# Kernel optimization log

Measured on AMD Instinct MI355X. Metric: run time of the kernel, lower is better.

## Reference

```python
import jax, jax.numpy as jnp
import numpy as np

B, NB, K, C, CM, POS = 8, 1024, 9, 32, 128, 2
SIGMA = 0.5
NEG_SLOPE = 0.01  # nn.LeakyReLU default
BN_EPS = 1e-5


def _leaky(x):
    return jnp.where(x >= 0, x, NEG_SLOPE * x)


def _batchnorm(x, gamma, beta):
    # BatchNorm1d, training-mode batch statistics over the point dimension
    mu = jnp.mean(x, axis=0)
    var = jnp.mean((x - mu) ** 2, axis=0)
    return gamma * (x - mu) * jax.lax.rsqrt(var + BN_EPS) + beta


def setup_inputs() -> dict:
    key = jax.random.key(0)
    ks = jax.random.split(key, 8)
    N = B * NB
    positions = jax.random.normal(ks[0], (N, POS), jnp.float32)
    weights = jax.random.normal(ks[1], (N, C), jnp.float32)
    batch = jnp.full((B,), NB, dtype=jnp.int32)  # uniform point counts per graph
    # KernelConv params: kernel_init='grid' -> 3x3 grid of offsets spanning +-sigma
    g = jnp.linspace(-SIGMA, SIGMA, 3, dtype=jnp.float32)
    kernel_positions = jnp.stack(jnp.meshgrid(g, g, indexing='ij'), axis=-1).reshape(K, POS)
    kernel_weights = (jax.random.normal(ks[2], (K, C, C), jnp.float32) / np.float32(np.sqrt(C * K)))
    conv_norm_gamma = jnp.ones((C,), jnp.float32)
    conv_norm_beta = jnp.zeros((C,), jnp.float32)
    # PyG MLP([C, CM, C+POS], act_first=True, plain_last=True)
    W1 = jax.random.normal(ks[3], (C, CM), jnp.float32) / np.float32(np.sqrt(C))
    b1 = jnp.zeros((CM,), jnp.float32)
    bn_gamma = jnp.ones((CM,), jnp.float32)
    bn_beta = jnp.zeros((CM,), jnp.float32)
    W2 = jax.random.normal(ks[4], (CM, C + POS), jnp.float32) / np.float32(np.sqrt(CM))
    b2 = jnp.zeros((C + POS,), jnp.float32)
    return dict(positions=positions, weights=weights, batch=batch,
                kernel_positions=kernel_positions, kernel_weights=kernel_weights,
                conv_norm_gamma=conv_norm_gamma, conv_norm_beta=conv_norm_beta,
                W1=W1, b1=b1, bn_gamma=bn_gamma, bn_beta=bn_beta, W2=W2, b2=b2)


def reference(positions, weights, batch, kernel_positions, kernel_weights,
              conv_norm_gamma, conv_norm_beta, W1, b1, bn_gamma, bn_beta, W2, b2):
    N = positions.shape[0]
    # --- KernelConv: each point spawns K components at pos + kernel offset ---
    conv_pos = (positions[:, None, :] + kernel_positions[None, :, :])  # [N,K,2]
    conv_w = jnp.einsum('nc,kcd->nkd', weights, kernel_weights)        # [N,K,C]
    conv_pos = conv_pos.reshape(B, NB * K, POS)
    conv_w = conv_w.reshape(B, NB * K, C)
    # --- KernelSample: evaluate Gaussian mixture at original positions ---
    p = positions.reshape(B, NB, POS)
    d2 = (jnp.sum(p * p, -1)[:, :, None]
          + jnp.sum(conv_pos * conv_pos, -1)[:, None, :]
          - 2.0 * jnp.einsum('bnd,bmd->bnm', p, conv_pos))             # [B,NB,NB*K]
    Kmat = jnp.exp(-d2 / (2.0 * SIGMA * SIGMA))
    sampled = jnp.einsum('bnm,bmc->bnc', Kmat, conv_w).reshape(N, C)
    x = _leaky(sampled)                                                 # KernelSample nonlinearity
    # conv_norm + residual add of input weights
    x = _batchnorm(x, conv_norm_gamma, conv_norm_beta) + weights
    # MLP: lin -> act -> batchnorm (act_first) -> plain last lin
    h = _batchnorm(_leaky(x @ W1 + b1), bn_gamma, bn_beta)
    mlp_out = h @ W2 + b2                                               # [N, POS + C]
    delta_pos, delta_w = mlp_out[:, :POS], mlp_out[:, POS:]
    return positions + delta_pos, x + delta_w
```

## Files before the change

### kernel.cpp

```cpp
#include <hip/hip_runtime.h>
#include <hip/hip_bf16.h>

#define BB    8
#define NBB   1024
#define KK    9
#define CC    32
#define CMM   128
#define NTOT  (BB*NBB)
#define MM    (NBB*KK)
#define NEG   0.01f
#define EPS   1e-5f
#define SQL2  1.6986436f

#define OFF_CWT   0
#define SZ_CWT    (BB*CC*MM/2)
#define OFF_QPX   (OFF_CWT + SZ_CWT)
#define OFF_QPY   (OFF_QPX + BB*MM)
#define OFF_X0    (OFF_QPY + BB*MM)
#define OFF_X     (OFF_X0 + NTOT*CC)
#define OFF_H0    (OFF_X + NTOT*CC)
#define OFF_ST    (OFF_H0 + NTOT*CMM)

typedef __attribute__((ext_vector_type(8))) short short8;
typedef __attribute__((ext_vector_type(4))) float f32x4;
typedef __attribute__((ext_vector_type(2))) float f32x2;

static __device__ __forceinline__ unsigned short f2bf_rne(float f) {
    __hip_bfloat16 h = __float2bfloat16(f);
    return *reinterpret_cast<unsigned short*>(&h);
}


__global__ __launch_bounds__(256) void k_convw(const float* __restrict__ pos,
                                               const float* __restrict__ kpos,
                                               const float* __restrict__ w,
                                               const float* __restrict__ kw,
                                               float* __restrict__ qpx,
                                               float* __restrict__ qpy,
                                               float* __restrict__ stats,
                                               short* __restrict__ cwT) {
    __shared__ unsigned short kwl[KK*CC*CC];
    __shared__ unsigned short tile[9*32*32];
    int t = threadIdx.x;
    int l = t & 63, wv = t >> 6;
    int lane15 = l & 15, quad = l >> 4;
    int blk = blockIdx.x;
    int b = blk & 7, nbl = blk >> 3;

    if (blk == 0 && t < 320) stats[t] = 0.f;
    #pragma unroll
    for (int rep = 0; rep < 2; ++rep) {
        int gid = rep*65536 + blk*256 + t;
        if (gid < BB*MM) {
            int bb = gid / MM;
            int m = gid - bb*MM;
            int np = m / 9, k9 = m - np*9;
            float qx = pos[((size_t)(bb*NBB + np))*2 + 0] + kpos[k9*2 + 0];
            float qy = pos[((size_t)(bb*NBB + np))*2 + 1] + kpos[k9*2 + 1];
            qpx[gid] = SQL2*qx;
            qpy[gid] = SQL2*qy;
        }
    }
    for (int u = t; u < KK*CC*CC/4; u += 256) {
        int flat = u*4;
        int row = flat >> 5;
        int c0 = flat & 31;
        int kk = row >> 5, cp = row & 31;
        f32x4 v = *(const f32x4*)&kw[flat];
        kwl[(kk*CC + c0+0)*CC + cp] = f2bf_rne(v.x);
        kwl[(kk*CC + c0+1)*CC + cp] = f2bf_rne(v.y);
        kwl[(kk*CC + c0+2)*CC + cp] = f2bf_rne(v.z);
        kwl[(kk*CC + c0+3)*CC + cp] = f2bf_rne(v.w);
    }
    int n = b*NBB + nbl*32 + (wv & 1)*16 + lane15;
    f32x4 w0 = *(const f32x4*)&w[(size_t)n*CC + quad*8];
    f32x4 w1 = *(const f32x4*)&w[(size_t)n*CC + quad*8 + 4];
    union { unsigned short us[8]; short8 s; } bfr;
    bfr.us[0] = f2bf_rne(w0.x); bfr.us[1] = f2bf_rne(w0.y);
    bfr.us[2] = f2bf_rne(w0.z); bfr.us[3] = f2bf_rne(w0.w);
    bfr.us[4] = f2bf_rne(w1.x); bfr.us[5] = f2bf_rne(w1.y);
    bfr.us[6] = f2bf_rne(w1.z); bfr.us[7] = f2bf_rne(w1.w);
    __syncthreads();
    {
        int ntile = wv & 1, cth = wv >> 1;
        f32x4 acc[KK];
        #pragma unroll
        for (int kk = 0; kk < KK; ++kk) {
            int c = cth*16 + lane15;
            short8 afr = *(const short8*)&kwl[(kk*CC + c)*CC + quad*8];
            acc[kk] = __builtin_amdgcn_mfma_f32_16x16x32_bf16(
                afr, bfr.s, (f32x4)0.f, 0, 0, 0);
        }
        #pragma unroll
        for (int kk = 0; kk < KK; ++kk) {
            int ml = (ntile*16 + lane15)*9 + kk;
            unsigned short* tw = &tile[(ml >> 5)*1024 + (ml & 31)];
            #pragma unroll
            for (int reg = 0; reg < 4; ++reg) {
                int c = cth*16 + quad*4 + reg;
                tw[c*32] = f2bf_rne(acc[kk][reg]);
            }
        }
    }
    __syncthreads();
    short* dst = cwT + (size_t)b*CC*MM + (size_t)nbl*9216;
    #pragma unroll
    for (int it = 0; it < 5; ++it) {
        int u = it*256 + t;
        if (u < 1152) {
            short8 v = *(const short8*)&tile[u*8];
            *(short8*)&dst[u*8] = v;
        }
    }
}

#define LOADSET(A0,A1,XX0,XX1,YY0,YY1,it) do { \
    int _i = (it) < 18 ? (it) : 17; \
    int _m = wvm + _i*32; \
    int _a = _i*1024; \
    A0 = *(const short8*)&cab[_a]; \
    A1 = *(const short8*)&cab[_a + 512]; \
    XX0 = *(const f32x4*)&qx[_m]; XX1 = *(const f32x4*)&qx[_m + 4]; \
    YY0 = *(const f32x4*)&qy[_m]; YY1 = *(const f32x4*)&qy[_m + 4]; \
} while (0)

#define COMPUTE(A0,A1,XX0,XX1,YY0,YY1) do { \
    _Pragma("unroll") \
    for (int nt = 0; nt < 2; ++nt) { \
        f32x2 PX = {px[nt], px[nt]}; \
        f32x2 PY = {py[nt], py[nt]}; \
        f32x2 dx0 = (f32x2){XX0.x, XX0.y} - PX; \
        f32x2 dy0 = (f32x2){YY0.x, YY0.y} - PY; \
        f32x2 t0 = dx0*dx0; t0 = dy0*dy0 + t0; \
        f32x2 dx1 = (f32x2){XX0.z, XX0.w} - PX; \
        f32x2 dy1 = (f32x2){YY0.z, YY0.w} - PY; \
        f32x2 t1 = dx1*dx1; t1 = dy1*dy1 + t1; \
        f32x2 dx2 = (f32x2){XX1.x, XX1.y} - PX; \
        f32x2 dy2 = (f32x2){YY1.x, YY1.y} - PY; \
        f32x2 t2 = dx2*dx2; t2 = dy2*dy2 + t2; \
        f32x2 dx3 = (f32x2){XX1.z, XX1.w} - PX; \
        f32x2 dy3 = (f32x2){YY1.z, YY1.w} - PY; \
        f32x2 t3 = dx3*dx3; t3 = dy3*dy3 + t3; \
        float e0 = __builtin_amdgcn_exp2f(-t0.x); \
        float e1 = __builtin_amdgcn_exp2f(-t0.y); \
        float e2 = __builtin_amdgcn_exp2f(-t1.x); \
        float e3 = __builtin_amdgcn_exp2f(-t1.y); \
        float e4 = __builtin_amdgcn_exp2f(-t2.x); \
        float e5 = __builtin_amdgcn_exp2f(-t2.y); \
        float e6 = __builtin_amdgcn_exp2f(-t3.x); \
        float e7 = __builtin_amdgcn_exp2f(-t3.y); \
        union { unsigned int u[4]; short8 s; } bf; \
        bf.u[0] = __builtin_amdgcn_perm(__float_as_uint(e1), __float_as_uint(e0), 0x07060302u); \
        bf.u[1] = __builtin_amdgcn_perm(__float_as_uint(e3), __float_as_uint(e2), 0x07060302u); \
        bf.u[2] = __builtin_amdgcn_perm(__float_as_uint(e5), __float_as_uint(e4), 0x07060302u); \
        bf.u[3] = __builtin_amdgcn_perm(__float_as_uint(e7), __float_as_uint(e6), 0x07060302u); \
        acc[nt][0] = __builtin_amdgcn_mfma_f32_16x16x32_bf16(A0, bf.s, acc[nt][0], 0, 0, 0); \
        acc[nt][1] = __builtin_amdgcn_mfma_f32_16x16x32_bf16(A1, bf.s, acc[nt][1], 0, 0, 0); \
    } \
} while (0)

__global__ __launch_bounds__(1024, 4) void k_sample(const float* __restrict__ pos,
                                                    const float* __restrict__ qpx,
                                                    const float* __restrict__ qpy,
                                                    const short* __restrict__ cwT,
                                                    float* __restrict__ x0,
                                                    float* __restrict__ s1) {
    __shared__ float red[16*32*36];
    __shared__ float sstat[64];
    int t = threadIdx.x;
    int l = t & 63, wv = t >> 6;
    int blk = blockIdx.x;
    int b = blk & 7, nblk = blk >> 3;
    int lane15 = l & 15, quad = l >> 4;
    int nbase = b*NBB + nblk*32;
    if (t < 64) sstat[t] = 0.f;

    float px[2], py[2];
    #pragma unroll
    for (int nt = 0; nt < 2; ++nt) {
        int n = nbase + nt*16 + lane15;
        px[nt] = SQL2*pos[(size_t)n*2];
        py[nt] = SQL2*pos[(size_t)n*2 + 1];
    }
    f32x4 acc[2][2];
    acc[0][0] = (f32x4)0.f; acc[0][1] = (f32x4)0.f;
    acc[1][0] = (f32x4)0.f; acc[1][1] = (f32x4)0.f;

    const float* qx = qpx + (size_t)b*MM;
    const float* qy = qpy + (size_t)b*MM;
    const short* cab = cwT + (size_t)b*CC*MM + (size_t)(wv*18)*1024
                     + (size_t)lane15*32 + quad*8;
    const int wvm = wv*576 + quad*8;

    short8 a0A, a1A, a0B, a1B, a0C, a1C;
    f32x4 X0A, X1A, Y0A, Y1A, X0B, X1B, Y0B, Y1B, X0C, X1C, Y0C, Y1C;
    LOADSET(a0A, a1A, X0A, X1A, Y0A, Y1A, 0);
    LOADSET(a0B, a1B, X0B, X1B, Y0B, Y1B, 1);
    LOADSET(a0C, a1C, X0C, X1C, Y0C, Y1C, 2);
    for (int i = 0; i < 6; ++i) {
        int base = i*3;
        COMPUTE(a0A, a1A, X0A, X1A, Y0A, Y1A);
        LOADSET(a0A, a1A, X0A, X1A, Y0A, Y1A, base + 3);
        COMPUTE(a0B, a1B, X0B, X1B, Y0B, Y1B);
        LOADSET(a0B, a1B, X0B, X1B, Y0B, Y1B, base + 4);
        COMPUTE(a0C, a1C, X0C, X1C, Y0C, Y1C);
        LOADSET(a0C, a1C, X0C, X1C, Y0C, Y1C, base + 5);
    }
    #pragma unroll
    for (int nt = 0; nt < 2; ++nt)
        #pragma unroll
        for (int ct = 0; ct < 2; ++ct) {
            int nn = nt*16 + lane15, c = ct*16 + quad*4;
            *(f32x4*)&red[(wv*32 + nn)*36 + c] = acc[nt][ct];
        }
    __syncthreads();
    if (t < 256) {
        int nr = t >> 3, c0 = (t & 7)*4;
        f32x4 v = (f32x4)0.f;
        #pragma unroll
        for (int wp = 0; wp < 16; ++wp)
            v = v + *(const f32x4*)&red[(wp*32 + nr)*36 + c0];
        v.x = v.x >= 0.f ? v.x : NEG*v.x;
        v.y = v.y >= 0.f ? v.y : NEG*v.y;
        v.z = v.z >= 0.f ? v.z : NEG*v.z;
        v.w = v.w >= 0.f ? v.w : NEG*v.w;
        *(f32x4*)&x0[((size_t)(nbase + nr))*CC + c0] = v;
        float s0 = v.x, s1v = v.y, s2v = v.z, s3v = v.w;
        float q0 = v.x*v.x, q1 = v.y*v.y, q2 = v.z*v.z, q3 = v.w*v.w;
        #pragma unroll
        for (int mk = 8; mk <= 32; mk <<= 1) {
            s0 += __shfl_xor(s0, mk); s1v += __shfl_xor(s1v, mk);
            s2v += __shfl_xor(s2v, mk); s3v += __shfl_xor(s3v, mk);
            q0 += __shfl_xor(q0, mk); q1 += __shfl_xor(q1, mk);
            q2 += __shfl_xor(q2, mk); q3 += __shfl_xor(q3, mk);
        }
        if (l < 8) {
            atomicAdd(&sstat[c0 + 0], s0);  atomicAdd(&sstat[c0 + 1], s1v);
            atomicAdd(&sstat[c0 + 2], s2v); atomicAdd(&sstat[c0 + 3], s3v);
            atomicAdd(&sstat[32 + c0 + 0], q0); atomicAdd(&sstat[32 + c0 + 1], q1);
            atomicAdd(&sstat[32 + c0 + 2], q2); atomicAdd(&sstat[32 + c0 + 3], q3);
        }
    }
    __syncthreads();
    if (t < 64) atomicAdd(&s1[t], sstat[t]);
}

__global__ __launch_bounds__(256) void k_mlp1(const float* __restrict__ x0,
                                              const float* __restrict__ wts,
                                              const float* __restrict__ gma,
                                              const float* __restrict__ bta,
                                              const float* __restrict__ W1,
                                              const float* __restrict__ b1,
                                              const float* __restrict__ s1,
                                              float* __restrict__ x,
                                              float* __restrict__ h0,
                                              float* __restrict__ s2) {
    __shared__ float tile[32*68];
    int t = threadIdx.x;
    int l = t & 63, wv = t >> 6;
    int blk = blockIdx.x;
    int nb = blk >> 2, jq = blk & 3;
    int n = nb*64 + l;
    int j0 = jq*32 + wv*8;

    float xv[32];
    #pragma unroll
    for (int c = 0; c < 32; ++c) {
        float mu  = s1[c] * (1.f/NTOT);
        float var = s1[32+c]*(1.f/NTOT) - mu*mu;
        float a   = gma[c] * rsqrtf(var + EPS);
        float v   = x0[(size_t)n*CC + c];
        xv[c] = a*(v - mu) + bta[c] + wts[(size_t)n*CC + c];
    }
    if (jq == 0 && wv == 0) {
        #pragma unroll
        for (int c = 0; c < 32; c += 4)
            *(float4*)&x[(size_t)n*CC + c] = make_float4(xv[c], xv[c+1], xv[c+2], xv[c+3]);
    }
    float acc[8];
    *(f32x4*)&acc[0] = *(const f32x4*)&b1[j0];
    *(f32x4*)&acc[4] = *(const f32x4*)&b1[j0 + 4];
    #pragma unroll 8
    for (int c = 0; c < 32; ++c) {
        float xc = xv[c];
        const float* w1r = W1 + c*CMM + j0;
        f32x4 wa = *(const f32x4*)&w1r[0];
        f32x4 wb = *(const f32x4*)&w1r[4];
        acc[0] = fmaf(xc, wa.x, acc[0]); acc[1] = fmaf(xc, wa.y, acc[1]);
        acc[2] = fmaf(xc, wa.z, acc[2]); acc[3] = fmaf(xc, wa.w, acc[3]);
        acc[4] = fmaf(xc, wb.x, acc[4]); acc[5] = fmaf(xc, wb.y, acc[5]);
        acc[6] = fmaf(xc, wb.z, acc[6]); acc[7] = fmaf(xc, wb.w, acc[7]);
    }
    #pragma unroll
    for (int jj = 0; jj < 8; ++jj) {
        acc[jj] = acc[jj] >= 0.f ? acc[jj] : NEG*acc[jj];
        tile[(wv*8 + jj)*68 + l] = acc[jj];
    }
    float* hd = h0 + (size_t)n*CMM + j0;
    *(float4*)&hd[0] = make_float4(acc[0], acc[1], acc[2], acc[3]);
    *(float4*)&hd[4] = make_float4(acc[4], acc[5], acc[6], acc[7]);
    __syncthreads();
    if (t < 256) {
        int jl = t >> 3, grp = t & 7;
        float lsum = 0.f, lsq = 0.f;
        #pragma unroll
        for (int q = 0; q < 2; ++q) {
            f32x4 v = *(const f32x4*)&tile[jl*68 + grp*8 + q*4];
            lsum += v.x + v.y + v.z + v.w;
            lsq = fmaf(v.x, v.x, fmaf(v.y, v.y, fmaf(v.z, v.z, fmaf(v.w, v.w, lsq))));
        }
        lsum += __shfl_xor(lsum, 1); lsq += __shfl_xor(lsq, 1);
        lsum += __shfl_xor(lsum, 2); lsq += __shfl_xor(lsq, 2);
        lsum += __shfl_xor(lsum, 4); lsq += __shfl_xor(lsq, 4);
        if (grp == 0) {
            int jg = jq*32 + jl;
            atomicAdd(&s2[jg], lsum);
            atomicAdd(&s2[CMM + jg], lsq);
        }
    }
}

__global__ __launch_bounds__(256) void k_mlp2(const float* __restrict__ h0,
                                              const float* __restrict__ x,
                                              const float* __restrict__ pos,
                                              const float* __restrict__ g2,
                                              const float* __restrict__ bt2,
                                              const float* __restrict__ W2,
                                              const float* __restrict__ b2,
                                              const float* __restrict__ s2,
                                              float* __restrict__ out) {
    __shared__ float red[16*16*35];
    int t = threadIdx.x;
    int nl = t & 15, rid = t >> 4;
    int n = blockIdx.x*16 + nl;
    int j0 = rid*8;
    float hv[8];
    *(f32x4*)&hv[0] = *(const f32x4*)&h0[(size_t)n*CMM + j0];
    *(f32x4*)&hv[4] = *(const f32x4*)&h0[(size_t)n*CMM + j0 + 4];
    #pragma unroll
    for (int jj = 0; jj < 8; ++jj) {
        int j = j0 + jj;
        float mu  = s2[j] * (1.f/NTOT);
        float var = s2[CMM+j]*(1.f/NTOT) - mu*mu;
        float a   = g2[j] * rsqrtf(var + EPS);
        hv[jj] = a*(hv[jj] - mu) + bt2[j];
    }
    float acc[34];
    #pragma unroll
    for (int c = 0; c < 34; ++c) acc[c] = 0.f;
    for (int jj = 0; jj < 8; ++jj) {
        float h = hv[jj];
        const float* w2r = W2 + (size_t)(j0 + jj)*34;
        #pragma unroll
        for (int c = 0; c < 34; ++c)
            acc[c] = fmaf(h, w2r[c], acc[c]);
    }
    #pragma unroll
    for (int c = 0; c < 34; ++c) red[(rid*16 + nl)*35 + c] = acc[c];
    __syncthreads();
    #pragma unroll
    for (int it = 0; it < 3; ++it) {
        int u = it*256 + t;
        if (u < 544) {
            int r = u / 34, c = u - r*34;
            float v = b2[c];
            #pragma unroll
            for (int rr = 0; rr < 16; ++rr) v += red[(rr*16 + r)*35 + c];
            int nn = blockIdx.x*16 + r;
            if (c < 2)
                out[(size_t)nn*2 + c] = pos[(size_t)nn*2 + c] + v;
            else
                out[16384 + (size_t)nn*32 + (c-2)] = x[(size_t)nn*32 + (c-2)] + v;
        }
    }
}

extern "C" void kernel_launch(void* const* d_in, const int* in_sizes, int n_in,
                              void* d_out, int out_size, void* d_ws, size_t ws_size,
                              hipStream_t stream) {
    const float* positions = (const float*)d_in[0];
    const float* weights   = (const float*)d_in[1];
    const float* kpos = (const float*)d_in[3];
    const float* kw   = (const float*)d_in[4];
    const float* cg   = (const float*)d_in[5];
    const float* cb   = (const float*)d_in[6];
    const float* W1   = (const float*)d_in[7];
    const float* b1   = (const float*)d_in[8];
    const float* bg   = (const float*)d_in[9];
    const float* bb   = (const float*)d_in[10];
    const float* W2   = (const float*)d_in[11];
    const float* b2   = (const float*)d_in[12];
    float* ws  = (float*)d_ws;
    float* out = (float*)d_out;

    float* s1 = ws + OFF_ST;
    float* s2 = ws + OFF_ST + 64;

    k_convw<<<256, 256, 0, stream>>>(positions, kpos, weights, kw,
                                     ws + OFF_QPX, ws + OFF_QPY,
                                     s1, (short*)(ws + OFF_CWT));
    k_sample<<<256, 1024, 0, stream>>>(positions, ws + OFF_QPX, ws + OFF_QPY,
                                       (const short*)(ws + OFF_CWT),
                                       ws + OFF_X0, s1);
    k_mlp1<<<512, 256, 0, stream>>>(ws + OFF_X0, weights, cg, cb, W1, b1,
                                    s1, ws + OFF_X, ws + OFF_H0, s2);
    k_mlp2<<<512, 256, 0, stream>>>(ws + OFF_H0, ws + OFF_X, positions,
                                    bg, bb, W2, b2, s2, out);
}
```

Measured before the change: 145.0 us.

## Fuse four kernels into two using software grid barriers

Merges the conv-weight precompute into the sampling kernel and the two MLP kernels into one, separated by a hand-rolled atomic grid barrier. This removes two kernel launches and their launch gaps. In exchange it depends on every block being co-resident (256 blocks of 1024 threads, and 512 blocks of 256), since the barrier deadlocks otherwise. The spin-wait also adds some cost.

```diff
diff --git a/kernel.cpp b/kernel.cpp
--- a/kernel.cpp
+++ b/kernel.cpp
@@ -30,89 +30,27 @@
     return *reinterpret_cast<unsigned short*>(&h);
 }
 
-
-__global__ __launch_bounds__(256) void k_convw(const float* __restrict__ pos,
-                                               const float* __restrict__ kpos,
-                                               const float* __restrict__ w,
-                                               const float* __restrict__ kw,
-                                               float* __restrict__ qpx,
-                                               float* __restrict__ qpy,
-                                               float* __restrict__ stats,
-                                               short* __restrict__ cwT) {
-    __shared__ unsigned short kwl[KK*CC*CC];
-    __shared__ unsigned short tile[9*32*32];
-    int t = threadIdx.x;
-    int l = t & 63, wv = t >> 6;
-    int lane15 = l & 15, quad = l >> 4;
-    int blk = blockIdx.x;
-    int b = blk & 7, nbl = blk >> 3;
-
-    if (blk == 0 && t < 320) stats[t] = 0.f;
-    #pragma unroll
-    for (int rep = 0; rep < 2; ++rep) {
-        int gid = rep*65536 + blk*256 + t;
-        if (gid < BB*MM) {
-            int bb = gid / MM;
-            int m = gid - bb*MM;
-            int np = m / 9, k9 = m - np*9;
-            float qx = pos[((size_t)(bb*NBB + np))*2 + 0] + kpos[k9*2 + 0];
-            float qy = pos[((size_t)(bb*NBB + np))*2 + 1] + kpos[k9*2 + 1];
-            qpx[gid] = SQL2*qx;
-            qpy[gid] = SQL2*qy;
-        }
-    }
-    for (int u = t; u < KK*CC*CC/4; u += 256) {
-        int flat = u*4;
-        int row = flat >> 5;
-        int c0 = flat & 31;
-        int kk = row >> 5, cp = row & 31;
-        f32x4 v = *(const f32x4*)&kw[flat];
-        kwl[(kk*CC + c0+0)*CC + cp] = f2bf_rne(v.x);
-        kwl[(kk*CC + c0+1)*CC + cp] = f2bf_rne(v.y);
-        kwl[(kk*CC + c0+2)*CC + cp] = f2bf_rne(v.z);
-        kwl[(kk*CC + c0+3)*CC + cp] = f2bf_rne(v.w);
-    }
-    int n = b*NBB + nbl*32 + (wv & 1)*16 + lane15;
-    f32x4 w0 = *(const f32x4*)&w[(size_t)n*CC + quad*8];
-    f32x4 w1 = *(const f32x4*)&w[(size_t)n*CC + quad*8 + 4];
-    union { unsigned short us[8]; short8 s; } bfr;
-    bfr.us[0] = f2bf_rne(w0.x); bfr.us[1] = f2bf_rne(w0.y);
-    bfr.us[2] = f2bf_rne(w0.z); bfr.us[3] = f2bf_rne(w0.w);
-    bfr.us[4] = f2bf_rne(w1.x); bfr.us[5] = f2bf_rne(w1.y);
-    bfr.us[6] = f2bf_rne(w1.z); bfr.us[7] = f2bf_rne(w1.w);
+__device__ unsigned g_cnt[2];
+__device__ unsigned g_gen[2];
+
+static __device__ __forceinline__ void grid_sync(int i, unsigned nblk) {
+    __threadfence();
     __syncthreads();
-    {
-        int ntile = wv & 1, cth = wv >> 1;
-        f32x4 acc[KK];
-        #pragma unroll
-        for (int kk = 0; kk < KK; ++kk) {
-            int c = cth*16 + lane15;
-            short8 afr = *(const short8*)&kwl[(kk*CC + c)*CC + quad*8];
-            acc[kk] = __builtin_amdgcn_mfma_f32_16x16x32_bf16(
-                afr, bfr.s, (f32x4)0.f, 0, 0, 0);
-        }
-        #pragma unroll
-        for (int kk = 0; kk < KK; ++kk) {
-            int ml = (ntile*16 + lane15)*9 + kk;
-            unsigned short* tw = &tile[(ml >> 5)*1024 + (ml & 31)];
-            #pragma unroll
-            for (int reg = 0; reg < 4; ++reg) {
-                int c = cth*16 + quad*4 + reg;
-                tw[c*32] = f2bf_rne(acc[kk][reg]);
-            }
+    if (threadIdx.x == 0) {
+        unsigned g = __hip_atomic_load(&g_gen[i], __ATOMIC_RELAXED, __HIP_MEMORY_SCOPE_AGENT);
+        unsigned a = __hip_atomic_fetch_add(&g_cnt[i], 1u, __ATOMIC_ACQ_REL, __HIP_MEMORY_SCOPE_AGENT);
+        if (a == nblk - 1u) {
+            __hip_atomic_store(&g_cnt[i], 0u, __ATOMIC_RELAXED, __HIP_MEMORY_SCOPE_AGENT);
+            __hip_atomic_store(&g_gen[i], g + 1u, __ATOMIC_RELEASE, __HIP_MEMORY_SCOPE_AGENT);
+        } else {
+            while (__hip_atomic_load(&g_gen[i], __ATOMIC_ACQUIRE, __HIP_MEMORY_SCOPE_AGENT) == g)
+                __builtin_amdgcn_s_sleep(2);
         }
     }
     __syncthreads();
-    short* dst = cwT + (size_t)b*CC*MM + (size_t)nbl*9216;
-    #pragma unroll
-    for (int it = 0; it < 5; ++it) {
-        int u = it*256 + t;
-        if (u < 1152) {
-            short8 v = *(const short8*)&tile[u*8];
-            *(short8*)&dst[u*8] = v;
-        }
-    }
+    __threadfence();
 }
+
 
 #define LOADSET(A0,A1,XX0,XX1,YY0,YY1,it) do { \
     int _i = (it) < 18 ? (it) : 17; \
@@ -159,218 +97,299 @@
     } \
 } while (0)
 
-__global__ __launch_bounds__(1024, 4) void k_sample(const float* __restrict__ pos,
-                                                    const float* __restrict__ qpx,
-                                                    const float* __restrict__ qpy,
-                                                    const short* __restrict__ cwT,
-                                                    float* __restrict__ x0,
-                                                    float* __restrict__ s1) {
+__global__ __launch_bounds__(1024, 4) void k_cs(const float* __restrict__ pos,
+                                                const float* __restrict__ kpos,
+                                                const float* __restrict__ w,
+                                                const float* __restrict__ kw,
+                                                float* __restrict__ qpx,
+                                                float* __restrict__ qpy,
+                                                const short* __restrict__ cwTr,
+                                                short* __restrict__ cwT,
+                                                float* __restrict__ x0,
+                                                float* __restrict__ stats) {
     __shared__ float red[16*32*36];
     __shared__ float sstat[64];
+    unsigned short* kwl  = (unsigned short*)red;
+    unsigned short* tile = (unsigned short*)red + 9216;
+
     int t = threadIdx.x;
     int l = t & 63, wv = t >> 6;
     int blk = blockIdx.x;
     int b = blk & 7, nblk = blk >> 3;
     int lane15 = l & 15, quad = l >> 4;
-    int nbase = b*NBB + nblk*32;
     if (t < 64) sstat[t] = 0.f;
 
-    float px[2], py[2];
-    #pragma unroll
-    for (int nt = 0; nt < 2; ++nt) {
-        int n = nbase + nt*16 + lane15;
-        px[nt] = SQL2*pos[(size_t)n*2];
-        py[nt] = SQL2*pos[(size_t)n*2 + 1];
-    }
-    f32x4 acc[2][2];
-    acc[0][0] = (f32x4)0.f; acc[0][1] = (f32x4)0.f;
-    acc[1][0] = (f32x4)0.f; acc[1][1] = (f32x4)0.f;
-
-    const float* qx = qpx + (size_t)b*MM;
-    const float* qy = qpy + (size_t)b*MM;
-    const short* cab = cwT + (size_t)b*CC*MM + (size_t)(wv*18)*1024
-                     + (size_t)lane15*32 + quad*8;
-    const int wvm = wv*576 + quad*8;
-
-    short8 a0A, a1A, a0B, a1B, a0C, a1C;
-    f32x4 X0A, X1A, Y0A, Y1A, X0B, X1B, Y0B, Y1B, X0C, X1C, Y0C, Y1C;
-    LOADSET(a0A, a1A, X0A, X1A, Y0A, Y1A, 0);
-    LOADSET(a0B, a1B, X0B, X1B, Y0B, Y1B, 1);
-    LOADSET(a0C, a1C, X0C, X1C, Y0C, Y1C, 2);
-    for (int i = 0; i < 6; ++i) {
-        int base = i*3;
-        COMPUTE(a0A, a1A, X0A, X1A, Y0A, Y1A);
-        LOADSET(a0A, a1A, X0A, X1A, Y0A, Y1A, base + 3);
-        COMPUTE(a0B, a1B, X0B, X1B, Y0B, Y1B);
-        LOADSET(a0B, a1B, X0B, X1B, Y0B, Y1B, base + 4);
-        COMPUTE(a0C, a1C, X0C, X1C, Y0C, Y1C);
-        LOADSET(a0C, a1C, X0C, X1C, Y0C, Y1C, base + 5);
-    }
-    #pragma unroll
-    for (int nt = 0; nt < 2; ++nt)
-        #pragma unroll
-        for (int ct = 0; ct < 2; ++ct) {
-            int nn = nt*16 + lane15, c = ct*16 + quad*4;
-            *(f32x4*)&red[(wv*32 + nn)*36 + c] = acc[nt][ct];
-        }
+    if (blk == 0 && t < 320) stats[t] = 0.f;
+    {
+        int gid = blk*1024 + t;
+        if (gid < BB*MM) {
+            int bb = gid / MM;
+            int m = gid - bb*MM;
+            int np = m / 9, k9 = m - np*9;
+            float qxv = pos[((size_t)(bb*NBB + np))*2 + 0] + kpos[k9*2 + 0];
+            float qyv = pos[((size_t)(bb*NBB + np))*2 + 1] + kpos[k9*2 + 1];
+            qpx[gid] = SQL2*qxv;
+            qpy[gid] = SQL2*qyv;
+        }
+    }
+    for (int u = t; u < KK*CC*CC/4; u += 1024) {
+        int flat = u*4;
+        int row = flat >> 5;
+        int c0 = flat & 31;
+        int kk = row >> 5, cp = row & 31;
+        f32x4 v = *(const f32x4*)&kw[flat];
+        kwl[(kk*CC + c0+0)*CC + cp] = f2bf_rne(v.x);
+        kwl[(kk*CC + c0+1)*CC + cp] = f2bf_rne(v.y);
+        kwl[(kk*CC + c0+2)*CC + cp] = f2bf_rne(v.z);
+        kwl[(kk*CC + c0+3)*CC + cp] = f2bf_rne(v.w);
+    }
+    {
+        int n = b*NBB + nblk*32 + (wv & 1)*16 + lane15;
+        f32x4 w0 = *(const f32x4*)&w[(size_t)n*CC + quad*8];
+        f32x4 w1 = *(const f32x4*)&w[(size_t)n*CC + quad*8 + 4];
+        union { unsigned short us[8]; short8 s; } bfr;
+        bfr.us[0] = f2bf_rne(w0.x); bfr.us[1] = f2bf_rne(w0.y);
+        bfr.us[2] = f2bf_rne(w0.z); bfr.us[3] = f2bf_rne(w0.w);
+        bfr.us[4] = f2bf_rne(w1.x); bfr.us[5] = f2bf_rne(w1.y);
+        bfr.us[6] = f2bf_rne(w1.z); bfr.us[7] = f2bf_rne(w1.w);
+        __syncthreads();
+        if (wv < 4) {
+            int ntile = wv & 1, cth = wv >> 1;
+            f32x4 acw[KK];
+            #pragma unroll
+            for (int kk = 0; kk < KK; ++kk) {
+                int c = cth*16 + lane15;
+                short8 afr = *(const short8*)&kwl[(kk*CC + c)*CC + quad*8];
+                acw[kk] = __builtin_amdgcn_mfma_f32_16x16x32_bf16(
+                    afr, bfr.s, (f32x4)0.f, 0, 0, 0);
+            }
+            #pragma unroll
+            for (int kk = 0; kk < KK; ++kk) {
+                int ml = (ntile*16 + lane15)*9 + kk;
+                unsigned short* tw = &tile[(ml >> 5)*1024 + (ml & 31)];
+                #pragma unroll
+                for (int reg = 0; reg < 4; ++reg) {
+                    int c = cth*16 + quad*4 + reg;
+                    tw[c*32] = f2bf_rne(acw[kk][reg]);
+                }
+            }
+        }
+    }
     __syncthreads();
-    if (t < 256) {
-        int nr = t >> 3, c0 = (t & 7)*4;
-        f32x4 v = (f32x4)0.f;
-        #pragma unroll
-        for (int wp = 0; wp < 16; ++wp)
-            v = v + *(const f32x4*)&red[(wp*32 + nr)*36 + c0];
-        v.x = v.x >= 0.f ? v.x : NEG*v.x;
-        v.y = v.y >= 0.f ? v.y : NEG*v.y;
-        v.z = v.z >= 0.f ? v.z : NEG*v.z;
-        v.w = v.w >= 0.f ? v.w : NEG*v.w;
-        *(f32x4*)&x0[((size_t)(nbase + nr))*CC + c0] = v;
-        float s0 = v.x, s1v = v.y, s2v = v.z, s3v = v.w;
-        float q0 = v.x*v.x, q1 = v.y*v.y, q2 = v.z*v.z, q3 = v.w*v.w;
-        #pragma unroll
-        for (int mk = 8; mk <= 32; mk <<= 1) {
-            s0 += __shfl_xor(s0, mk); s1v += __shfl_xor(s1v, mk);
-            s2v += __shfl_xor(s2v, mk); s3v += __shfl_xor(s3v, mk);
-            q0 += __shfl_xor(q0, mk); q1 += __shfl_xor(q1, mk);
-            q2 += __shfl_xor(q2, mk); q3 += __shfl_xor(q3, mk);
-        }
-        if (l < 8) {
-            atomicAdd(&sstat[c0 + 0], s0);  atomicAdd(&sstat[c0 + 1], s1v);
-            atomicAdd(&sstat[c0 + 2], s2v); atomicAdd(&sstat[c0 + 3], s3v);
-            atomicAdd(&sstat[32 + c0 + 0], q0); atomicAdd(&sstat[32 + c0 + 1], q1);
-            atomicAdd(&sstat[32 + c0 + 2], q2); atomicAdd(&sstat[32 + c0 + 3], q3);
-        }
-    }
-    __syncthreads();
-    if (t < 64) atomicAdd(&s1[t], sstat[t]);
+    {
+        short* dst = cwT + (size_t)b*CC*MM + (size_t)nblk*9216;
+        #pragma unroll
+        for (int it = 0; it < 2; ++it) {
+            int u = it*1024 + t;
+            if (u < 1152) {
+                short8 v = *(const short8*)&tile[u*8];
+                *(short8*)&dst[u*8] = v;
+            }
+        }
+    }
+    grid_sync(0, 256);
+
+    {
+        int nbase = b*NBB + nblk*32;
+        float px[2], py[2];
+        #pragma unroll
+        for (int nt = 0; nt < 2; ++nt) {
+            int n = nbase + nt*16 + lane15;
+            px[nt] = SQL2*pos[(size_t)n*2];
+            py[nt] = SQL2*pos[(size_t)n*2 + 1];
+        }
+        f32x4 acc[2][2];
+        acc[0][0] = (f32x4)0.f; acc[0][1] = (f32x4)0.f;
+        acc[1][0] = (f32x4)0.f; acc[1][1] = (f32x4)0.f;
+
+        const float* qx = qpx + (size_t)b*MM;
+        const float* qy = qpy + (size_t)b*MM;
+        const short* cab = cwTr + (size_t)b*CC*MM + (size_t)(wv*18)*1024
+                         + (size_t)lane15*32 + quad*8;
+        const int wvm = wv*576 + quad*8;
+
+        short8 a0A, a1A, a0B, a1B, a0C, a1C;
+        f32x4 X0A, X1A, Y0A, Y1A, X0B, X1B, Y0B, Y1B, X0C, X1C, Y0C, Y1C;
+        LOADSET(a0A, a1A, X0A, X1A, Y0A, Y1A, 0);
+        LOADSET(a0B, a1B, X0B, X1B, Y0B, Y1B, 1);
+        LOADSET(a0C, a1C, X0C, X1C, Y0C, Y1C, 2);
+        for (int i = 0; i < 6; ++i) {
+            int base = i*3;
+            COMPUTE(a0A, a1A, X0A, X1A, Y0A, Y1A);
+            LOADSET(a0A, a1A, X0A, X1A, Y0A, Y1A, base + 3);
+            COMPUTE(a0B, a1B, X0B, X1B, Y0B, Y1B);
+            LOADSET(a0B, a1B, X0B, X1B, Y0B, Y1B, base + 4);
+            COMPUTE(a0C, a1C, X0C, X1C, Y0C, Y1C);
+            LOADSET(a0C, a1C, X0C, X1C, Y0C, Y1C, base + 5);
+        }
+        #pragma unroll
+        for (int nt = 0; nt < 2; ++nt)
+            #pragma unroll
+            for (int ct = 0; ct < 2; ++ct) {
+                int nn = nt*16 + lane15, c = ct*16 + quad*4;
+                *(f32x4*)&red[(wv*32 + nn)*36 + c] = acc[nt][ct];
+            }
+        __syncthreads();
+        if (t < 256) {
+            int nr = t >> 3, c0 = (t & 7)*4;
+            f32x4 v = (f32x4)0.f;
+            #pragma unroll
+            for (int wp = 0; wp < 16; ++wp)
+                v = v + *(const f32x4*)&red[(wp*32 + nr)*36 + c0];
+            v.x = v.x >= 0.f ? v.x : NEG*v.x;
+            v.y = v.y >= 0.f ? v.y : NEG*v.y;
+            v.z = v.z >= 0.f ? v.z : NEG*v.z;
+            v.w = v.w >= 0.f ? v.w : NEG*v.w;
+            *(f32x4*)&x0[((size_t)(nbase + nr))*CC + c0] = v;
+            float s0 = v.x, s1v = v.y, s2v = v.z, s3v = v.w;
+            float q0 = v.x*v.x, q1 = v.y*v.y, q2 = v.z*v.z, q3 = v.w*v.w;
+            #pragma unroll
+            for (int mk = 8; mk <= 32; mk <<= 1) {
+                s0 += __shfl_xor(s0, mk); s1v += __shfl_xor(s1v, mk);
+                s2v += __shfl_xor(s2v, mk); s3v += __shfl_xor(s3v, mk);
+                q0 += __shfl_xor(q0, mk); q1 += __shfl_xor(q1, mk);
+                q2 += __shfl_xor(q2, mk); q3 += __shfl_xor(q3, mk);
+            }
+            if (l < 8) {
+                atomicAdd(&sstat[c0 + 0], s0);  atomicAdd(&sstat[c0 + 1], s1v);
+                atomicAdd(&sstat[c0 + 2], s2v); atomicAdd(&sstat[c0 + 3], s3v);
+                atomicAdd(&sstat[32 + c0 + 0], q0); atomicAdd(&sstat[32 + c0 + 1], q1);
+                atomicAdd(&sstat[32 + c0 + 2], q2); atomicAdd(&sstat[32 + c0 + 3], q3);
+            }
+        }
+        __syncthreads();
+        if (t < 64) atomicAdd(&stats[t], sstat[t]);
+    }
 }
 
-__global__ __launch_bounds__(256) void k_mlp1(const float* __restrict__ x0,
-                                              const float* __restrict__ wts,
-                                              const float* __restrict__ gma,
-                                              const float* __restrict__ bta,
-                                              const float* __restrict__ W1,
-                                              const float* __restrict__ b1,
-                                              const float* __restrict__ s1,
-                                              float* __restrict__ x,
-                                              float* __restrict__ h0,
-                                              float* __restrict__ s2) {
-    __shared__ float tile[32*68];
+__global__ __launch_bounds__(256) void k_mlp(const float* __restrict__ x0,
+                                             const float* __restrict__ wts,
+                                             const float* __restrict__ gma,
+                                             const float* __restrict__ bta,
+                                             const float* __restrict__ W1,
+                                             const float* __restrict__ b1,
+                                             const float* __restrict__ s1,
+                                             float* __restrict__ x,
+                                             float* __restrict__ h0,
+                                             float* __restrict__ s2,
+                                             const float* __restrict__ pos,
+                                             const float* __restrict__ g2,
+                                             const float* __restrict__ bt2,
+                                             const float* __restrict__ W2,
+                                             const float* __restrict__ b2,
+                                             float* __restrict__ out) {
+    __shared__ float sm[16*16*35];
     int t = threadIdx.x;
     int l = t & 63, wv = t >> 6;
     int blk = blockIdx.x;
-    int nb = blk >> 2, jq = blk & 3;
-    int n = nb*64 + l;
-    int j0 = jq*32 + wv*8;
-
-    float xv[32];
-    #pragma unroll
-    for (int c = 0; c < 32; ++c) {
-        float mu  = s1[c] * (1.f/NTOT);
-        float var = s1[32+c]*(1.f/NTOT) - mu*mu;
-        float a   = gma[c] * rsqrtf(var + EPS);
-        float v   = x0[(size_t)n*CC + c];
-        xv[c] = a*(v - mu) + bta[c] + wts[(size_t)n*CC + c];
-    }
-    if (jq == 0 && wv == 0) {
-        #pragma unroll
-        for (int c = 0; c < 32; c += 4)
-            *(float4*)&x[(size_t)n*CC + c] = make_float4(xv[c], xv[c+1], xv[c+2], xv[c+3]);
-    }
-    float acc[8];
-    *(f32x4*)&acc[0] = *(const f32x4*)&b1[j0];
-    *(f32x4*)&acc[4] = *(const f32x4*)&b1[j0 + 4];
-    #pragma unroll 8
-    for (int c = 0; c < 32; ++c) {
-        float xc = xv[c];
-        const float* w1r = W1 + c*CMM + j0;
-        f32x4 wa = *(const f32x4*)&w1r[0];
-        f32x4 wb = *(const f32x4*)&w1r[4];
-        acc[0] = fmaf(xc, wa.x, acc[0]); acc[1] = fmaf(xc, wa.y, acc[1]);
-        acc[2] = fmaf(xc, wa.z, acc[2]); acc[3] = fmaf(xc, wa.w, acc[3]);
-        acc[4] = fmaf(xc, wb.x, acc[4]); acc[5] = fmaf(xc, wb.y, acc[5]);
-        acc[6] = fmaf(xc, wb.z, acc[6]); acc[7] = fmaf(xc, wb.w, acc[7]);
-    }
-    #pragma unroll
-    for (int jj = 0; jj < 8; ++jj) {
-        acc[jj] = acc[jj] >= 0.f ? acc[jj] : NEG*acc[jj];
-        tile[(wv*8 + jj)*68 + l] = acc[jj];
-    }
-    float* hd = h0 + (size_t)n*CMM + j0;
-    *(float4*)&hd[0] = make_float4(acc[0], acc[1], acc[2], acc[3]);
-    *(float4*)&hd[4] = make_float4(acc[4], acc[5], acc[6], acc[7]);
-    __syncthreads();
-    if (t < 256) {
-        int jl = t >> 3, grp = t & 7;
-        float lsum = 0.f, lsq = 0.f;
-        #pragma unroll
-        for (int q = 0; q < 2; ++q) {
-            f32x4 v = *(const f32x4*)&tile[jl*68 + grp*8 + q*4];
-            lsum += v.x + v.y + v.z + v.w;
-            lsq = fmaf(v.x, v.x, fmaf(v.y, v.y, fmaf(v.z, v.z, fmaf(v.w, v.w, lsq))));
-        }
-        lsum += __shfl_xor(lsum, 1); lsq += __shfl_xor(lsq, 1);
-        lsum += __shfl_xor(lsum, 2); lsq += __shfl_xor(lsq, 2);
-        lsum += __shfl_xor(lsum, 4); lsq += __shfl_xor(lsq, 4);
-        if (grp == 0) {
-            int jg = jq*32 + jl;
-            atomicAdd(&s2[jg], lsum);
-            atomicAdd(&s2[CMM + jg], lsq);
-        }
-    }
-}
-
-__global__ __launch_bounds__(256) void k_mlp2(const float* __restrict__ h0,
-                                              const float* __restrict__ x,
-                                              const float* __restrict__ pos,
-                                              const float* __restrict__ g2,
-                                              const float* __restrict__ bt2,
-                                              const float* __restrict__ W2,
-                                              const float* __restrict__ b2,
-                                              const float* __restrict__ s2,
-                                              float* __restrict__ out) {
-    __shared__ float red[16*16*35];
-    int t = threadIdx.x;
-    int nl = t & 15, rid = t >> 4;
-    int n = blockIdx.x*16 + nl;
-    int j0 = rid*8;
-    float hv[8];
-    *(f32x4*)&hv[0] = *(const f32x4*)&h0[(size_t)n*CMM + j0];
-    *(f32x4*)&hv[4] = *(const f32x4*)&h0[(size_t)n*CMM + j0 + 4];
-    #pragma unroll
-    for (int jj = 0; jj < 8; ++jj) {
-        int j = j0 + jj;
-        float mu  = s2[j] * (1.f/NTOT);
-        float var = s2[CMM+j]*(1.f/NTOT) - mu*mu;
-        float a   = g2[j] * rsqrtf(var + EPS);
-        hv[jj] = a*(hv[jj] - mu) + bt2[j];
-    }
-    float acc[34];
-    #pragma unroll
-    for (int c = 0; c < 34; ++c) acc[c] = 0.f;
-    for (int jj = 0; jj < 8; ++jj) {
-        float h = hv[jj];
-        const float* w2r = W2 + (size_t)(j0 + jj)*34;
-        #pragma unroll
-        for (int c = 0; c < 34; ++c)
-            acc[c] = fmaf(h, w2r[c], acc[c]);
-    }
-    #pragma unroll
-    for (int c = 0; c < 34; ++c) red[(rid*16 + nl)*35 + c] = acc[c];
-    __syncthreads();
-    #pragma unroll
-    for (int it = 0; it < 3; ++it) {
-        int u = it*256 + t;
-        if (u < 544) {
-            int r = u / 34, c = u - r*34;
-            float v = b2[c];
-            #pragma unroll
-            for (int rr = 0; rr < 16; ++rr) v += red[(rr*16 + r)*35 + c];
-            int nn = blockIdx.x*16 + r;
-            if (c < 2)
-                out[(size_t)nn*2 + c] = pos[(size_t)nn*2 + c] + v;
-            else
-                out[16384 + (size_t)nn*32 + (c-2)] = x[(size_t)nn*32 + (c-2)] + v;
+
+    {
+        float* tile = sm;
+        int nb = blk >> 2, jq = blk & 3;
+        int n = nb*64 + l;
+        int j0 = jq*32 + wv*8;
+
+        float xv[32];
+        #pragma unroll
+        for (int c = 0; c < 32; ++c) {
+            float mu  = s1[c] * (1.f/NTOT);
+            float var = s1[32+c]*(1.f/NTOT) - mu*mu;
+            float a   = gma[c] * rsqrtf(var + EPS);
+            float v   = x0[(size_t)n*CC + c];
+            xv[c] = a*(v - mu) + bta[c] + wts[(size_t)n*CC + c];
+        }
+        if (jq == 0 && wv == 0) {
+            #pragma unroll
+            for (int c = 0; c < 32; c += 4)
+                *(float4*)&x[(size_t)n*CC + c] = make_float4(xv[c], xv[c+1], xv[c+2], xv[c+3]);
+        }
+        float acc[8];
+        *(f32x4*)&acc[0] = *(const f32x4*)&b1[j0];
+        *(f32x4*)&acc[4] = *(const f32x4*)&b1[j0 + 4];
+        #pragma unroll 8
+        for (int c = 0; c < 32; ++c) {
+            float xc = xv[c];
+            const float* w1r = W1 + c*CMM + j0;
+            f32x4 wa = *(const f32x4*)&w1r[0];
+            f32x4 wb = *(const f32x4*)&w1r[4];
+            acc[0] = fmaf(xc, wa.x, acc[0]); acc[1] = fmaf(xc, wa.y, acc[1]);
+            acc[2] = fmaf(xc, wa.z, acc[2]); acc[3] = fmaf(xc, wa.w, acc[3]);
+            acc[4] = fmaf(xc, wb.x, acc[4]); acc[5] = fmaf(xc, wb.y, acc[5]);
+            acc[6] = fmaf(xc, wb.z, acc[6]); acc[7] = fmaf(xc, wb.w, acc[7]);
+        }
+        #pragma unroll
+        for (int jj = 0; jj < 8; ++jj) {
+            acc[jj] = acc[jj] >= 0.f ? acc[jj] : NEG*acc[jj];
+            tile[(wv*8 + jj)*68 + l] = acc[jj];
+        }
+        float* hd = h0 + (size_t)n*CMM + j0;
+        *(float4*)&hd[0] = make_float4(acc[0], acc[1], acc[2], acc[3]);
+        *(float4*)&hd[4] = make_float4(acc[4], acc[5], acc[6], acc[7]);
+        __syncthreads();
+        {
+            int jl = t >> 3, grp = t & 7;
+            float lsum = 0.f, lsq = 0.f;
+            #pragma unroll
+            for (int q = 0; q < 2; ++q) {
+                f32x4 v = *(const f32x4*)&tile[jl*68 + grp*8 + q*4];
+                lsum += v.x + v.y + v.z + v.w;
+                lsq = fmaf(v.x, v.x, fmaf(v.y, v.y, fmaf(v.z, v.z, fmaf(v.w, v.w, lsq))));
+            }
+            lsum += __shfl_xor(lsum, 1); lsq += __shfl_xor(lsq, 1);
+            lsum += __shfl_xor(lsum, 2); lsq += __shfl_xor(lsq, 2);
+            lsum += __shfl_xor(lsum, 4); lsq += __shfl_xor(lsq, 4);
+            if (grp == 0) {
+                int jg = jq*32 + jl;
+                atomicAdd(&s2[jg], lsum);
+                atomicAdd(&s2[CMM + jg], lsq);
+            }
+        }
+    }
+    grid_sync(1, 512);
+
+    {
+        float* red = sm;
+        int nl = t & 15, rid = t >> 4;
+        int n = blk*16 + nl;
+        int j0 = rid*8;
+        float hv[8];
+        *(f32x4*)&hv[0] = *(const f32x4*)&h0[(size_t)n*CMM + j0];
+        *(f32x4*)&hv[4] = *(const f32x4*)&h0[(size_t)n*CMM + j0 + 4];
+        #pragma unroll
+        for (int jj = 0; jj < 8; ++jj) {
+            int j = j0 + jj;
+            float mu  = s2[j] * (1.f/NTOT);
+            float var = s2[CMM+j]*(1.f/NTOT) - mu*mu;
+            float a   = g2[j] * rsqrtf(var + EPS);
+            hv[jj] = a*(hv[jj] - mu) + bt2[j];
+        }
+        float acc[34];
+        #pragma unroll
+        for (int c = 0; c < 34; ++c) acc[c] = 0.f;
+        for (int jj = 0; jj < 8; ++jj) {
+            float h = hv[jj];
+            const float* w2r = W2 + (size_t)(j0 + jj)*34;
+            #pragma unroll
+            for (int c = 0; c < 34; ++c)
+                acc[c] = fmaf(h, w2r[c], acc[c]);
+        }
+        #pragma unroll
+        for (int c = 0; c < 34; ++c) red[(rid*16 + nl)*35 + c] = acc[c];
+        __syncthreads();
+        #pragma unroll
+        for (int it = 0; it < 3; ++it) {
+            int u = it*256 + t;
+            if (u < 544) {
+                int r = u / 34, c = u - r*34;
+                float v = b2[c];
+                #pragma unroll
+                for (int rr = 0; rr < 16; ++rr) v += red[(rr*16 + r)*35 + c];
+                int nn = blk*16 + r;
+                if (c < 2)
+                    out[(size_t)nn*2 + c] = pos[(size_t)nn*2 + c] + v;
+                else
+                    out[16384 + (size_t)nn*32 + (c-2)] = x[(size_t)nn*32 + (c-2)] + v;
+            }
         }
     }
 }
@@ -396,14 +415,12 @@
     float* s1 = ws + OFF_ST;
     float* s2 = ws + OFF_ST + 64;
 
-    k_convw<<<256, 256, 0, stream>>>(positions, kpos, weights, kw,
-                                     ws + OFF_QPX, ws + OFF_QPY,
-                                     s1, (short*)(ws + OFF_CWT));
-    k_sample<<<256, 1024, 0, stream>>>(positions, ws + OFF_QPX, ws + OFF_QPY,
-                                       (const short*)(ws + OFF_CWT),
-                                       ws + OFF_X0, s1);
-    k_mlp1<<<512, 256, 0, stream>>>(ws + OFF_X0, weights, cg, cb, W1, b1,
-                                    s1, ws + OFF_X, ws + OFF_H0, s2);
-    k_mlp2<<<512, 256, 0, stream>>>(ws + OFF_H0, ws + OFF_X, positions,
-                                    bg, bb, W2, b2, s2, out);
+    k_cs<<<256, 1024, 0, stream>>>(positions, kpos, weights, kw,
+                                   ws + OFF_QPX, ws + OFF_QPY,
+                                   (const short*)(ws + OFF_CWT),
+                                   (short*)(ws + OFF_CWT),
+                                   ws + OFF_X0, s1);
+    k_mlp<<<512, 256, 0, stream>>>(ws + OFF_X0, weights, cg, cb, W1, b1,
+                                   s1, ws + OFF_X, ws + OFF_H0, s2,
+                                   positions, bg, bb, W2, b2, out);
 }
```

Result: slower. 436.8 us (+201.3%).
